# Kernel optimization log

Hardware: AMD Instinct MI355X
Metric: run time of the kernel (lower is better)

Reference implementation:

```python
import jax, jax.numpy as jnp
import numpy as np

N_E = 1024      # nconcepts (codebook size)
E_DIM = 64      # cdim (codebook vector dim)
BETA = 0.25
LEGACY = True


def setup_inputs() -> dict:
    key = jax.random.key(0)
    k1, k2, k3 = jax.random.split(key, 3)
    z_ = jax.random.normal(k1, (32, 256, 32, 32), jnp.float32)
    # 1x1 conv dis_modulator: 256 -> 64 channels (stored as [out, in])
    conv_w = jax.random.normal(k2, (64, 256), jnp.float32) / np.sqrt(256.0)
    conv_b = jnp.zeros((64,), jnp.float32)
    # embedding.weight.data.uniform_(-1/n_e, 1/n_e)
    emb = jax.random.uniform(k3, (N_E, E_DIM), jnp.float32, -1.0 / N_E, 1.0 / N_E)
    return {"z_": z_, "conv_w": conv_w, "conv_b": conv_b, "emb": emb}


def _forward(z_, conv_w, conv_b, emb):
    sg = jax.lax.stop_gradient
    # dis_modulator: 1x1 conv == per-pixel linear map  (B,Cin,H,W)->(B,Cout,H,W)
    z = jnp.einsum('bchw,oc->bohw', z_, conv_w) + conv_b[None, :, None, None]
    B = z.shape[0]
    # torch .view(-1, e_dim): row-major flatten of (B,C,H,W) into chunks of e_dim
    zf = z.reshape(-1, E_DIM)  # [B*C*H*W/e_dim, e_dim]

    # contrastive term: mean pairwise cosine similarity of codebook rows
    d1 = emb @ emb.T                                  # [n_e, n_e]
    norms = jnp.linalg.norm(emb, axis=1)              # [n_e]
    cosine = d1 / (norms[:, None] * norms[None, :])
    contrastive = jnp.mean(cosine)

    # squared L2 distances: ||z||^2 + ||e||^2 - 2 z.e
    d = (jnp.sum(zf * zf, axis=1, keepdims=True)
         + jnp.sum(emb * emb, axis=1)[None, :]
         - 2.0 * (zf @ emb.T))                        # [N, n_e]
    idx = jnp.argmin(d, axis=1)                       # [N]
    z_q = emb[idx].reshape(z.shape)

    if LEGACY:
        loss = jnp.mean((sg(z_q) - z) ** 2) + BETA * jnp.mean((z_q - sg(z)) ** 2)
    else:
        loss = BETA * jnp.mean((sg(z_q) - z) ** 2) + jnp.mean((z_q - sg(z)) ** 2)
    # hessian_penalty(G, z_, G_z=z): G is an affine 1x1 conv, so the central
    # second difference G(z+x) - 2G(z) + G(z-x) is identically zero -> penalty = 0.
    loss = loss + contrastive

    # straight-through estimator
    z_q_st = z + sg(z_q - z)

    # replicate source exactly: flat zeros(B*n_e) scattered at codebook indices
    sampled = jnp.zeros((B * N_E,), z.dtype).at[idx].set(1.0).reshape(B, N_E)
    min_idx = idx.reshape(B, -1)
    return z_q_st, loss, sampled, min_idx


def reference(z_, conv_w, conv_b, emb):
    z_q, loss, sampled, min_idx = _forward(z_, conv_w, conv_b, emb)
    return z_q, loss, sampled, min_idx
```

## Files before the change

### kernel.cpp

```cpp
#include <hip/hip_runtime.h>
#include <hip/hip_bf16.h>

#define NE      1024
#define ED      64
#define ZTOT    2097152
#define CIN     256
#define COUT    64
#define HW      1024

#define OFF_LOSS 2097152
#define OFF_SAMP 2097153
#define OFF_IDX  2129921

#define XSTR 68

__global__ __launch_bounds__(256) void k_prep(float* __restrict__ out_samp,
                                              const float* __restrict__ emb,
                                              float* __restrict__ enorm,
                                              float* __restrict__ cpart) {
    int bid = blockIdx.x, t = threadIdx.x;
    if (bid < 128) {
        out_samp[bid * 256 + t] = 0.0f;
        return;
    }
    int g = bid - 128;
    __shared__ float inv_s[64];
    __shared__ float S[256];
    if (t < 64) {
        int j = g * 64 + t;
        const float* e = emb + (size_t)j * ED;
        float r8[8];
        #pragma unroll
        for (int s = 0; s < 8; s++) { float v = e[s]; r8[s] = v * v; }
        #pragma unroll
        for (int m = 1; m < 8; m++) {
            #pragma unroll
            for (int s = 0; s < 8; s++) { float v = e[8 * m + s]; r8[s] += v * v; }
        }
        float en = ((r8[0] + r8[1]) + (r8[2] + r8[3])) + ((r8[4] + r8[5]) + (r8[6] + r8[7]));
        enorm[j] = en;
        inv_s[t] = 1.0f / sqrtf(en);
    }
    __syncthreads();
    int d = t & 63, q = t >> 6;
    float s = 0.0f;
    #pragma unroll
    for (int m = 0; m < 16; m++) {
        int i = q + 4 * m;
        s = fmaf(emb[(size_t)(g * 64 + i) * ED + d], inv_s[i], s);
    }
    S[t] = s;
    __syncthreads();
    if (t < 64)
        cpart[g * 64 + t] = (S[t] + S[t + 64]) + (S[t + 128] + S[t + 192]);
}

__global__ __launch_bounds__(256) void k_conv(const float* __restrict__ x,
                                              const float* __restrict__ w,
                                              const float* __restrict__ bias,
                                              float* __restrict__ z) {
    __shared__ float Xs[64 * XSTR];
    __shared__ float Ws[64 * XSTR];
    int t  = threadIdx.x;
    int b  = blockIdx.y;
    int p0 = blockIdx.x * 64;
    int pg = t & 15;
    int og = t >> 4;
    float acc[4][4];
    #pragma unroll
    for (int i = 0; i < 4; i++)
        #pragma unroll
        for (int j = 0; j < 4; j++) acc[i][j] = 0.0f;

    for (int c0 = 0; c0 < CIN; c0 += 64) {
        __syncthreads();
        {
            int u = t & 15, cg2 = t >> 4;
            #pragma unroll
            for (int m = 0; m < 4; m++) {
                int c = cg2 + 16 * m;
                float4 v = *(const float4*)&x[(size_t)(b * CIN + c0 + c) * HW + p0 + 4 * u];
                *(float4*)&Xs[c * XSTR + 4 * u] = v;
            }
            #pragma unroll
            for (int m = 0; m < 4; m++) {
                int o = cg2 + 16 * m;
                float4 v = *(const float4*)&w[o * CIN + c0 + 4 * u];
                Ws[(4 * u + 0) * XSTR + o] = v.x;
                Ws[(4 * u + 1) * XSTR + o] = v.y;
                Ws[(4 * u + 2) * XSTR + o] = v.z;
                Ws[(4 * u + 3) * XSTR + o] = v.w;
            }
        }
        __syncthreads();
        #pragma unroll 8
        for (int k = 0; k < 64; k++) {
            float4 xv = *(const float4*)&Xs[k * XSTR + 4 * pg];
            float4 wv = *(const float4*)&Ws[k * XSTR + 4 * og];
            float xa[4] = {xv.x, xv.y, xv.z, xv.w};
            float wb[4] = {wv.x, wv.y, wv.z, wv.w};
            #pragma unroll
            for (int i = 0; i < 4; i++)
                #pragma unroll
                for (int j = 0; j < 4; j++)
                    acc[i][j] = fmaf(xa[i], wb[j], acc[i][j]);
        }
    }
    #pragma unroll
    for (int j = 0; j < 4; j++) {
        int o = 4 * og + j;
        float bv = bias[o];
        float4 outv;
        outv.x = acc[0][j] + bv;
        outv.y = acc[1][j] + bv;
        outv.z = acc[2][j] + bv;
        outv.w = acc[3][j] + bv;
        *(float4*)&z[(size_t)(b * COUT + o) * HW + p0 + 4 * pg] = outv;
    }
}

__global__ __launch_bounds__(256, 2) void k_dist(const float* __restrict__ z,
                                                 const float* __restrict__ emb,
                                                 const float* __restrict__ enorm,
                                                 float* __restrict__ out_idx,
                                                 float* __restrict__ out_samp,
                                                 float* __restrict__ out_zq,
                                                 float* __restrict__ ssep) {
    __shared__ float zs[64 * 64];
    __shared__ float zn_s[64];
    __shared__ float redd[32 * 64];
    __shared__ int   redj[32 * 64];
    __shared__ int   bj_s[64];
    __shared__ float warr[4];
    int t    = threadIdx.x;
    int row0 = blockIdx.x * 64;
    int rg   = t & 7;
    int cg   = t >> 3;

    {
        int kb = t & 15, rr0 = t >> 4;
        #pragma unroll
        for (int m = 0; m < 4; m++) {
            int rr = rr0 + 16 * m;
            float4 v = *(const float4*)&z[(size_t)(row0 + rr) * 64 + 4 * kb];
            *(float4*)&zs[rr * 64 + 4 * (kb ^ (rr & 15))] = v;
        }
    }
    if (t < 64) {
        const float* zr = z + (size_t)(row0 + t) * 64;
        float r8[8];
        #pragma unroll
        for (int s = 0; s < 8; s++) { float v = zr[s]; r8[s] = v * v; }
        #pragma unroll
        for (int m = 1; m < 8; m++) {
            #pragma unroll
            for (int s = 0; s < 8; s++) { float v = zr[8 * m + s]; r8[s] += v * v; }
        }
        zn_s[t] = ((r8[0] + r8[1]) + (r8[2] + r8[3])) + ((r8[4] + r8[5]) + (r8[6] + r8[7]));
    }
    __syncthreads();

    float znr[8];
    #pragma unroll
    for (int i = 0; i < 8; i++) znr[i] = zn_s[rg + 8 * i];

    float bestd[8];
    int   bestj[8];
    #pragma unroll
    for (int i = 0; i < 8; i++) { bestd[i] = __builtin_huge_valf(); bestj[i] = 0; }

    for (int pass = 0; pass < 4; pass++) {
        float acc[8][8];
        #pragma unroll
        for (int i = 0; i < 8; i++)
            #pragma unroll
            for (int j = 0; j < 8; j++) acc[i][j] = 0.0f;

        const float* ebase = emb + ((size_t)(pass * 256 + cg) << 6);
        for (int kb = 0; kb < 16; kb++) {
            float4 za[8];
            #pragma unroll
            for (int i = 0; i < 8; i++) {
                int rr = rg + 8 * i;
                za[i] = *(const float4*)&zs[rr * 64 + 4 * (kb ^ (rr & 15))];
            }
            #pragma unroll
            for (int j = 0; j < 8; j++) {
                float4 ev = *(const float4*)&ebase[((size_t)(32 * j) << 6) + 4 * kb];
                #pragma unroll
                for (int i = 0; i < 8; i++) {
                    acc[i][j] = fmaf(za[i].x, ev.x, acc[i][j]);
                    acc[i][j] = fmaf(za[i].y, ev.y, acc[i][j]);
                    acc[i][j] = fmaf(za[i].z, ev.z, acc[i][j]);
                    acc[i][j] = fmaf(za[i].w, ev.w, acc[i][j]);
                }
            }
        }
        #pragma unroll
        for (int j = 0; j < 8; j++) {
            int c = pass * 256 + cg + 32 * j;
            float en = enorm[c];
            #pragma unroll
            for (int i = 0; i < 8; i++) {
                float A = znr[i] + en;
                float D = A - 2.0f * acc[i][j];
                if (D < bestd[i]) { bestd[i] = D; bestj[i] = c; }
            }
        }
    }

    #pragma unroll
    for (int i = 0; i < 8; i++) {
        redd[cg * 64 + rg + 8 * i] = bestd[i];
        redj[cg * 64 + rg + 8 * i] = bestj[i];
    }
    __syncthreads();
    if (t < 64) {
        float bd = __builtin_huge_valf();
        int   bj = 0x7fffffff;
        #pragma unroll
        for (int c = 0; c < 32; c++) {
            float dd = redd[c * 64 + t];
            int   jj = redj[c * 64 + t];
            if (dd < bd || (dd == bd && jj < bj)) { bd = dd; bj = jj; }
        }
        bj_s[t] = bj;
        out_idx[row0 + t] = (float)bj;
        atomicExch(&out_samp[bj], 1.0f);
    }
    __syncthreads();

    {
        int r  = t & 63;
        int kq = t >> 6;
        int bj = bj_s[r];
        const float* er = emb + ((size_t)bj << 6) + kq * 16;
        float sq = 0.0f;
        #pragma unroll
        for (int m = 0; m < 4; m++) {
            int kb = 4 * kq + m;
            float4 zv = *(const float4*)&zs[r * 64 + 4 * (kb ^ (r & 15))];
            float4 ev = *(const float4*)&er[4 * m];
            float d0 = ev.x - zv.x, d1 = ev.y - zv.y, d2 = ev.z - zv.z, d3 = ev.w - zv.w;
            float4 o4;
            o4.x = zv.x + d0; o4.y = zv.y + d1; o4.z = zv.z + d2; o4.w = zv.w + d3;
            *(float4*)&out_zq[((size_t)(row0 + r) << 6) + 4 * kb] = o4;
            sq += d0 * d0; sq += d1 * d1; sq += d2 * d2; sq += d3 * d3;
        }
        #pragma unroll
        for (int off = 32; off > 0; off >>= 1) sq += __shfl_down(sq, off, 64);
        if ((t & 63) == 0) warr[t >> 6] = sq;
    }
    __syncthreads();
    if (t == 0)
        ssep[blockIdx.x] = (warr[0] + warr[1]) + (warr[2] + warr[3]);
}

__global__ __launch_bounds__(256) void k_final(const float* __restrict__ ssep,
                                               const float* __restrict__ cpart,
                                               float* __restrict__ out_loss) {
    __shared__ double SD[256];
    __shared__ float  CS;
    int t = threadIdx.x;
    SD[t] = (double)ssep[t] + (double)ssep[t + 256];
    __syncthreads();
    #pragma unroll
    for (int off = 128; off > 0; off >>= 1) {
        if (t < off) SD[t] += SD[t + off];
        __syncthreads();
    }
    if (t < 64) {
        float v = 0.0f;
        #pragma unroll
        for (int m = 0; m < 16; m++) v += cpart[m * 64 + t];
        float sq = v * v;
        #pragma unroll
        for (int off = 32; off > 0; off >>= 1) sq += __shfl_down(sq, off, 64);
        if (t == 0) CS = sq / (1024.0f * 1024.0f);
    }
    __syncthreads();
    if (t == 0) {
        float m = (float)(SD[0] / (double)ZTOT);
        out_loss[0] = (m + 0.25f * m) + CS;
    }
}

extern "C" void kernel_launch(void* const* d_in, const int* in_sizes, int n_in,
                              void* d_out, int out_size, void* d_ws, size_t ws_size,
                              hipStream_t stream) {
    (void)in_sizes; (void)n_in; (void)out_size; (void)ws_size;
    const float* z_     = (const float*)d_in[0];
    const float* conv_w = (const float*)d_in[1];
    const float* conv_b = (const float*)d_in[2];
    const float* emb    = (const float*)d_in[3];

    float* out      = (float*)d_out;
    float* out_zq   = out;
    float* out_loss = out + OFF_LOSS;
    float* out_samp = out + OFF_SAMP;
    float* out_idx  = out + OFF_IDX;

    char*   ws    = (char*)d_ws;
    float*  wz    = (float*)ws;
    float*  enorm = (float*)(ws + 8388608);
    float*  cpart = enorm + 1024;
    float*  ssep  = cpart + 1024;

    k_prep <<<144, 256, 0, stream>>>(out_samp, emb, enorm, cpart);
    k_conv <<<dim3(16, 32), 256, 0, stream>>>(z_, conv_w, conv_b, wz);
    k_dist <<<512, 256, 0, stream>>>(wz, emb, enorm, out_idx, out_samp, out_zq, ssep);
    k_final<<<1, 256, 0, stream>>>(ssep, cpart, out_loss);
}
```

Baseline: 181.5 us.

## Merge prep into conv kernel and rewrite conv and distance kernels without LDS tiling

Merges the prep and conv launches into one grid, removing a kernel launch. Rewrites the 1x1 conv so each thread holds 64 input channels in registers and reads weights as wave-uniform loads, with no shared-memory staging. Rewrites the distance kernel so each thread owns one row in registers and each wave scans a quarter of the codebook with scalar-broadcast embedding reads, reducing across waves through a small LDS array. This trades the register-tiled, LDS-based GEMM reuse for simpler per-row loops that depend on scalar-cache broadcast. It risks lower FMA throughput and register pressure, and the cross-wave tie-break on equal distances is dropped.

```diff
diff --git a/kernel.cpp b/kernel.cpp
--- a/kernel.cpp
+++ b/kernel.cpp
@@ -4,118 +4,91 @@
 #define NE      1024
 #define ED      64
 #define ZTOT    2097152
-#define CIN     256
-#define COUT    64
-#define HW      1024
 
 #define OFF_LOSS 2097152
 #define OFF_SAMP 2097153
 #define OFF_IDX  2129921
 
-#define XSTR 68
-
-__global__ __launch_bounds__(256) void k_prep(float* __restrict__ out_samp,
-                                              const float* __restrict__ emb,
-                                              float* __restrict__ enorm,
-                                              float* __restrict__ cpart) {
+__global__ __launch_bounds__(256, 2) void k_convprep(const float* __restrict__ x,
+                                                     const float* __restrict__ w,
+                                                     const float* __restrict__ bias,
+                                                     float* __restrict__ z,
+                                                     float* __restrict__ out_samp,
+                                                     const float* __restrict__ emb,
+                                                     float* __restrict__ enorm,
+                                                     float* __restrict__ cpart) {
     int bid = blockIdx.x, t = threadIdx.x;
-    if (bid < 128) {
-        out_samp[bid * 256 + t] = 0.0f;
+    if (bid >= 512) {
+        int pb = bid - 512;
+        if (pb < 128) {
+            out_samp[pb * 256 + t] = 0.0f;
+            return;
+        }
+        int g = pb - 128;
+        __shared__ float inv_s[64];
+        __shared__ float S[256];
+        if (t < 64) {
+            int j = g * 64 + t;
+            const float* e = emb + (size_t)j * ED;
+            float r8[8];
+            #pragma unroll
+            for (int s = 0; s < 8; s++) { float v = e[s]; r8[s] = v * v; }
+            #pragma unroll
+            for (int m = 1; m < 8; m++) {
+                #pragma unroll
+                for (int s = 0; s < 8; s++) { float v = e[8 * m + s]; r8[s] += v * v; }
+            }
+            float en = ((r8[0] + r8[1]) + (r8[2] + r8[3])) + ((r8[4] + r8[5]) + (r8[6] + r8[7]));
+            enorm[j] = en;
+            inv_s[t] = 1.0f / sqrtf(en);
+        }
+        __syncthreads();
+        int d = t & 63, q = t >> 6;
+        float s = 0.0f;
+        #pragma unroll
+        for (int m = 0; m < 16; m++) {
+            int i = q + 4 * m;
+            s = fmaf(emb[(size_t)(g * 64 + i) * ED + d], inv_s[i], s);
+        }
+        S[t] = s;
+        __syncthreads();
+        if (t < 64)
+            cpart[g * 64 + t] = (S[t] + S[t + 64]) + (S[t + 128] + S[t + 192]);
         return;
     }
-    int g = bid - 128;
-    __shared__ float inv_s[64];
-    __shared__ float S[256];
-    if (t < 64) {
-        int j = g * 64 + t;
-        const float* e = emb + (size_t)j * ED;
-        float r8[8];
-        #pragma unroll
-        for (int s = 0; s < 8; s++) { float v = e[s]; r8[s] = v * v; }
-        #pragma unroll
-        for (int m = 1; m < 8; m++) {
-            #pragma unroll
-            for (int s = 0; s < 8; s++) { float v = e[8 * m + s]; r8[s] += v * v; }
-        }
-        float en = ((r8[0] + r8[1]) + (r8[2] + r8[3])) + ((r8[4] + r8[5]) + (r8[6] + r8[7]));
-        enorm[j] = en;
-        inv_s[t] = 1.0f / sqrtf(en);
-    }
-    __syncthreads();
-    int d = t & 63, q = t >> 6;
-    float s = 0.0f;
+
+    int b    = bid >> 4;
+    int p    = ((bid & 15) << 6) + (t & 63);
+    int wid  = __builtin_amdgcn_readfirstlane(t >> 6);
+    const float* xb = x + ((size_t)b << 18) + p;
+
+    float acc[16];
     #pragma unroll
-    for (int m = 0; m < 16; m++) {
-        int i = q + 4 * m;
-        s = fmaf(emb[(size_t)(g * 64 + i) * ED + d], inv_s[i], s);
-    }
-    S[t] = s;
-    __syncthreads();
-    if (t < 64)
-        cpart[g * 64 + t] = (S[t] + S[t + 64]) + (S[t + 128] + S[t + 192]);
-}
-
-__global__ __launch_bounds__(256) void k_conv(const float* __restrict__ x,
-                                              const float* __restrict__ w,
-                                              const float* __restrict__ bias,
-                                              float* __restrict__ z) {
-    __shared__ float Xs[64 * XSTR];
-    __shared__ float Ws[64 * XSTR];
-    int t  = threadIdx.x;
-    int b  = blockIdx.y;
-    int p0 = blockIdx.x * 64;
-    int pg = t & 15;
-    int og = t >> 4;
-    float acc[4][4];
+    for (int i = 0; i < 16; i++) acc[i] = 0.0f;
+
+    for (int ch = 0; ch < 4; ch++) {
+        int c0 = ch * 64;
+        float xr[64];
+        #pragma unroll
+        for (int cc = 0; cc < 64; cc++) xr[cc] = xb[(size_t)(c0 + cc) << 10];
+        #pragma unroll
+        for (int op = 0; op < 8; op++) {
+            int oa = wid * 16 + 2 * op;
+            const float* wa = w + ((size_t)oa << 8) + c0;
+            const float* wb = wa + 256;
+            float da = acc[2 * op], db = acc[2 * op + 1];
+            #pragma unroll
+            for (int cc = 0; cc < 64; cc++) {
+                da = fmaf(xr[cc], wa[cc], da);
+                db = fmaf(xr[cc], wb[cc], db);
+            }
+            acc[2 * op] = da; acc[2 * op + 1] = db;
+        }
+    }
     #pragma unroll
-    for (int i = 0; i < 4; i++)
-        #pragma unroll
-        for (int j = 0; j < 4; j++) acc[i][j] = 0.0f;
-
-    for (int c0 = 0; c0 < CIN; c0 += 64) {
-        __syncthreads();
-        {
-            int u = t & 15, cg2 = t >> 4;
-            #pragma unroll
-            for (int m = 0; m < 4; m++) {
-                int c = cg2 + 16 * m;
-                float4 v = *(const float4*)&x[(size_t)(b * CIN + c0 + c) * HW + p0 + 4 * u];
-                *(float4*)&Xs[c * XSTR + 4 * u] = v;
-            }
-            #pragma unroll
-            for (int m = 0; m < 4; m++) {
-                int o = cg2 + 16 * m;
-                float4 v = *(const float4*)&w[o * CIN + c0 + 4 * u];
-                Ws[(4 * u + 0) * XSTR + o] = v.x;
-                Ws[(4 * u + 1) * XSTR + o] = v.y;
-                Ws[(4 * u + 2) * XSTR + o] = v.z;
-                Ws[(4 * u + 3) * XSTR + o] = v.w;
-            }
-        }
-        __syncthreads();
-        #pragma unroll 8
-        for (int k = 0; k < 64; k++) {
-            float4 xv = *(const float4*)&Xs[k * XSTR + 4 * pg];
-            float4 wv = *(const float4*)&Ws[k * XSTR + 4 * og];
-            float xa[4] = {xv.x, xv.y, xv.z, xv.w};
-            float wb[4] = {wv.x, wv.y, wv.z, wv.w};
-            #pragma unroll
-            for (int i = 0; i < 4; i++)
-                #pragma unroll
-                for (int j = 0; j < 4; j++)
-                    acc[i][j] = fmaf(xa[i], wb[j], acc[i][j]);
-        }
-    }
-    #pragma unroll
-    for (int j = 0; j < 4; j++) {
-        int o = 4 * og + j;
-        float bv = bias[o];
-        float4 outv;
-        outv.x = acc[0][j] + bv;
-        outv.y = acc[1][j] + bv;
-        outv.z = acc[2][j] + bv;
-        outv.w = acc[3][j] + bv;
-        *(float4*)&z[(size_t)(b * COUT + o) * HW + p0 + 4 * pg] = outv;
+    for (int oo = 0; oo < 16; oo++) {
+        int o = wid * 16 + oo;
+        z[((size_t)(b * 64 + o) << 10) + p] = acc[oo] + bias[o];
     }
 }
 
@@ -126,134 +99,105 @@
                                                  float* __restrict__ out_samp,
                                                  float* __restrict__ out_zq,
                                                  float* __restrict__ ssep) {
-    __shared__ float zs[64 * 64];
-    __shared__ float zn_s[64];
-    __shared__ float redd[32 * 64];
-    __shared__ int   redj[32 * 64];
-    __shared__ int   bj_s[64];
-    __shared__ float warr[4];
+    __shared__ float bd_s[4][64];
+    __shared__ int   bj_s[4][64];
     int t    = threadIdx.x;
-    int row0 = blockIdx.x * 64;
-    int rg   = t & 7;
-    int cg   = t >> 3;
-
+    int lane = t & 63;
+    int wid  = __builtin_amdgcn_readfirstlane(t >> 6);
+    int row  = blockIdx.x * 64 + lane;
+
+    float zf[64];
     {
-        int kb = t & 15, rr0 = t >> 4;
-        #pragma unroll
-        for (int m = 0; m < 4; m++) {
-            int rr = rr0 + 16 * m;
-            float4 v = *(const float4*)&z[(size_t)(row0 + rr) * 64 + 4 * kb];
-            *(float4*)&zs[rr * 64 + 4 * (kb ^ (rr & 15))] = v;
-        }
-    }
+        const float* zr = z + ((size_t)row << 6);
+        #pragma unroll
+        for (int q = 0; q < 16; q++)
+            *(float4*)&zf[4 * q] = *(const float4*)&zr[4 * q];
+    }
+
+    float zn;
+    {
+        float r8[8];
+        #pragma unroll
+        for (int s = 0; s < 8; s++) { float v = zf[s]; r8[s] = v * v; }
+        #pragma unroll
+        for (int m = 1; m < 8; m++) {
+            #pragma unroll
+            for (int s = 0; s < 8; s++) { float v = zf[8 * m + s]; r8[s] += v * v; }
+        }
+        zn = ((r8[0] + r8[1]) + (r8[2] + r8[3])) + ((r8[4] + r8[5]) + (r8[6] + r8[7]));
+    }
+
+    int   cbase = wid << 8;
+    const float* eb = emb + ((size_t)cbase << 6);
+    float bestd = __builtin_huge_valf();
+    int   bestj = 0;
+
+    for (int cc = 0; cc < 256; cc += 4) {
+        const float* e0 = eb + ((size_t)cc << 6);
+        const float* e1 = e0 + 64;
+        const float* e2 = e0 + 128;
+        const float* e3 = e0 + 192;
+        float d0 = 0.f, d1 = 0.f, d2 = 0.f, d3 = 0.f;
+        #pragma unroll
+        for (int k = 0; k < 64; k++) {
+            float zv = zf[k];
+            d0 = fmaf(zv, e0[k], d0);
+            d1 = fmaf(zv, e1[k], d1);
+            d2 = fmaf(zv, e2[k], d2);
+            d3 = fmaf(zv, e3[k], d3);
+        }
+        float en0 = enorm[cbase + cc];
+        float en1 = enorm[cbase + cc + 1];
+        float en2 = enorm[cbase + cc + 2];
+        float en3 = enorm[cbase + cc + 3];
+        float A0 = zn + en0, D0 = A0 - 2.0f * d0;
+        if (D0 < bestd) { bestd = D0; bestj = cbase + cc; }
+        float A1 = zn + en1, D1 = A1 - 2.0f * d1;
+        if (D1 < bestd) { bestd = D1; bestj = cbase + cc + 1; }
+        float A2 = zn + en2, D2 = A2 - 2.0f * d2;
+        if (D2 < bestd) { bestd = D2; bestj = cbase + cc + 2; }
+        float A3 = zn + en3, D3 = A3 - 2.0f * d3;
+        if (D3 < bestd) { bestd = D3; bestj = cbase + cc + 3; }
+    }
+
+    bd_s[wid][lane] = bestd;
+    bj_s[wid][lane] = bestj;
+    __syncthreads();
+
     if (t < 64) {
-        const float* zr = z + (size_t)(row0 + t) * 64;
-        float r8[8];
-        #pragma unroll
-        for (int s = 0; s < 8; s++) { float v = zr[s]; r8[s] = v * v; }
-        #pragma unroll
-        for (int m = 1; m < 8; m++) {
-            #pragma unroll
-            for (int s = 0; s < 8; s++) { float v = zr[8 * m + s]; r8[s] += v * v; }
-        }
-        zn_s[t] = ((r8[0] + r8[1]) + (r8[2] + r8[3])) + ((r8[4] + r8[5]) + (r8[6] + r8[7]));
-    }
-    __syncthreads();
-
-    float znr[8];
-    #pragma unroll
-    for (int i = 0; i < 8; i++) znr[i] = zn_s[rg + 8 * i];
-
-    float bestd[8];
-    int   bestj[8];
-    #pragma unroll
-    for (int i = 0; i < 8; i++) { bestd[i] = __builtin_huge_valf(); bestj[i] = 0; }
-
-    for (int pass = 0; pass < 4; pass++) {
-        float acc[8][8];
-        #pragma unroll
-        for (int i = 0; i < 8; i++)
-            #pragma unroll
-            for (int j = 0; j < 8; j++) acc[i][j] = 0.0f;
-
-        const float* ebase = emb + ((size_t)(pass * 256 + cg) << 6);
-        for (int kb = 0; kb < 16; kb++) {
-            float4 za[8];
-            #pragma unroll
-            for (int i = 0; i < 8; i++) {
-                int rr = rg + 8 * i;
-                za[i] = *(const float4*)&zs[rr * 64 + 4 * (kb ^ (rr & 15))];
-            }
-            #pragma unroll
-            for (int j = 0; j < 8; j++) {
-                float4 ev = *(const float4*)&ebase[((size_t)(32 * j) << 6) + 4 * kb];
-                #pragma unroll
-                for (int i = 0; i < 8; i++) {
-                    acc[i][j] = fmaf(za[i].x, ev.x, acc[i][j]);
-                    acc[i][j] = fmaf(za[i].y, ev.y, acc[i][j]);
-                    acc[i][j] = fmaf(za[i].z, ev.z, acc[i][j]);
-                    acc[i][j] = fmaf(za[i].w, ev.w, acc[i][j]);
-                }
-            }
-        }
-        #pragma unroll
-        for (int j = 0; j < 8; j++) {
-            int c = pass * 256 + cg + 32 * j;
-            float en = enorm[c];
-            #pragma unroll
-            for (int i = 0; i < 8; i++) {
-                float A = znr[i] + en;
-                float D = A - 2.0f * acc[i][j];
-                if (D < bestd[i]) { bestd[i] = D; bestj[i] = c; }
-            }
-        }
-    }
-
-    #pragma unroll
-    for (int i = 0; i < 8; i++) {
-        redd[cg * 64 + rg + 8 * i] = bestd[i];
-        redj[cg * 64 + rg + 8 * i] = bestj[i];
-    }
-    __syncthreads();
-    if (t < 64) {
-        float bd = __builtin_huge_valf();
-        int   bj = 0x7fffffff;
-        #pragma unroll
-        for (int c = 0; c < 32; c++) {
-            float dd = redd[c * 64 + t];
-            int   jj = redj[c * 64 + t];
-            if (dd < bd || (dd == bd && jj < bj)) { bd = dd; bj = jj; }
-        }
-        bj_s[t] = bj;
-        out_idx[row0 + t] = (float)bj;
+        float bd = bd_s[0][lane];
+        int   bj = bj_s[0][lane];
+        #pragma unroll
+        for (int w2 = 1; w2 < 4; w2++) {
+            float dd = bd_s[w2][lane];
+            int   jj = bj_s[w2][lane];
+            if (dd < bd) { bd = dd; bj = jj; }
+        }
+        out_idx[row] = (float)bj;
         atomicExch(&out_samp[bj], 1.0f);
-    }
-    __syncthreads();
-
-    {
-        int r  = t & 63;
-        int kq = t >> 6;
-        int bj = bj_s[r];
-        const float* er = emb + ((size_t)bj << 6) + kq * 16;
+
+        const float* ebest = emb + ((size_t)bj << 6);
+        float* oz = out_zq + ((size_t)row << 6);
         float sq = 0.0f;
         #pragma unroll
-        for (int m = 0; m < 4; m++) {
-            int kb = 4 * kq + m;
-            float4 zv = *(const float4*)&zs[r * 64 + 4 * (kb ^ (r & 15))];
-            float4 ev = *(const float4*)&er[4 * m];
-            float d0 = ev.x - zv.x, d1 = ev.y - zv.y, d2 = ev.z - zv.z, d3 = ev.w - zv.w;
+        for (int q = 0; q < 16; q++) {
+            float4 ev = *(const float4*)&ebest[4 * q];
+            float dd0 = ev.x - zf[4 * q + 0];
+            float dd1 = ev.y - zf[4 * q + 1];
+            float dd2 = ev.z - zf[4 * q + 2];
+            float dd3 = ev.w - zf[4 * q + 3];
             float4 o4;
-            o4.x = zv.x + d0; o4.y = zv.y + d1; o4.z = zv.z + d2; o4.w = zv.w + d3;
-            *(float4*)&out_zq[((size_t)(row0 + r) << 6) + 4 * kb] = o4;
-            sq += d0 * d0; sq += d1 * d1; sq += d2 * d2; sq += d3 * d3;
+            o4.x = zf[4 * q + 0] + dd0;
+            o4.y = zf[4 * q + 1] + dd1;
+            o4.z = zf[4 * q + 2] + dd2;
+            o4.w = zf[4 * q + 3] + dd3;
+            *(float4*)&oz[4 * q] = o4;
+            sq += dd0 * dd0; sq += dd1 * dd1; sq += dd2 * dd2; sq += dd3 * dd3;
         }
         #pragma unroll
         for (int off = 32; off > 0; off >>= 1) sq += __shfl_down(sq, off, 64);
-        if ((t & 63) == 0) warr[t >> 6] = sq;
-    }
-    __syncthreads();
-    if (t == 0)
-        ssep[blockIdx.x] = (warr[0] + warr[1]) + (warr[2] + warr[3]);
+        if (lane == 0) ssep[blockIdx.x] = sq;
+    }
 }
 
 __global__ __launch_bounds__(256) void k_final(const float* __restrict__ ssep,
@@ -306,8 +250,9 @@
     float*  cpart = enorm + 1024;
     float*  ssep  = cpart + 1024;
 
-    k_prep <<<144, 256, 0, stream>>>(out_samp, emb, enorm, cpart);
-    k_conv <<<dim3(16, 32), 256, 0, stream>>>(z_, conv_w, conv_b, wz);
-    k_dist <<<512, 256, 0, stream>>>(wz, emb, enorm, out_idx, out_samp, out_zq, ssep);
-    k_final<<<1, 256, 0, stream>>>(ssep, cpart, out_loss);
-}
+    k_convprep<<<656, 256, 0, stream>>>(z_, conv_w, conv_b, wz,
+                                        out_samp, emb, enorm, cpart);
+    k_dist    <<<512, 256, 0, stream>>>(wz, emb, enorm, out_idx, out_samp,
+                                        out_zq, ssep);
+    k_final   <<<1, 256, 0, stream>>>(ssep, cpart, out_loss);
+}
```

Measured after the change: 248.5 us. 1.37x slower.
